# Kernel optimization log

Hardware: AMD Instinct MI355X
Metric: run time of the kernel (lower is better)

The kernel has to match this reference:

```python
import jax, jax.numpy as jnp
import numpy as np

N_USER = 100000
N_ITEM = 50000
N = N_USER + N_ITEM  # 150000 nodes
D = 64               # embedding_size
L = 3                # num_layers
E = 2000000          # edges
B = 8192             # batch of (user, item_p, item_n) triples
INT_W, POP_W, TIDE_W = 0.1, 0.1, 0.2


def setup_inputs() -> dict:
    key = jax.random.key(0)
    ks = jax.random.split(key, 10)
    stdv = 1.0 / np.sqrt(D)
    emb_int = jax.random.uniform(ks[0], (N, D), minval=-stdv, maxval=stdv, dtype=jnp.float32)
    emb_pop = jax.random.uniform(ks[1], (N, D), minval=-stdv, maxval=stdv, dtype=jnp.float32)
    q = jax.random.uniform(ks[2], (N_ITEM,), dtype=jnp.float32)
    b = jax.random.uniform(ks[3], (N_ITEM,), dtype=jnp.float32)
    user = jax.random.randint(ks[4], (B, 1), 0, N_USER)
    item_p = jax.random.randint(ks[5], (B, 1), 0, N_ITEM)
    item_n = jax.random.randint(ks[6], (B, 1), 0, N_ITEM)
    mask = jax.random.randint(ks[7], (B, 1), 0, 2).astype(bool)
    edge_src = jax.random.randint(ks[8], (E,), 0, N)
    edge_dst = jax.random.randint(ks[9], (E,), 0, N)
    return {"emb_int": emb_int, "emb_pop": emb_pop, "q": q, "b": b,
            "user": user, "item_p": item_p, "item_n": item_n, "mask": mask,
            "edge_src": edge_src, "edge_dst": edge_dst}


def reference(emb_int, emb_pop, q, b, user, item_p, item_n, mask, edge_src, edge_dst):
    # --- LightGCN symmetric normalization coefficients (per edge) ---
    ones = jnp.ones(edge_src.shape, emb_int.dtype)
    deg_out = jax.ops.segment_sum(ones, edge_src, num_segments=N)
    deg_in = jax.ops.segment_sum(ones, edge_dst, num_segments=N)
    norm = (jax.lax.rsqrt(jnp.maximum(deg_out, 1.0))[edge_src]
            * jax.lax.rsqrt(jnp.maximum(deg_in, 1.0))[edge_dst])  # [E]

    def propagate(e0):
        # L layers of LGConv (gather-scale-scatter), mean over layer outputs incl. layer 0.
        # Dropout is identity in eval mode (training=False).
        acc, h = e0, e0
        for _ in range(L):
            h = jax.ops.segment_sum(h[edge_src] * norm[:, None], edge_dst, num_segments=N)
            acc = acc + h
        return acc / (L + 1)

    f_int = propagate(emb_int)  # [N, D]
    f_pop = propagate(emb_pop)  # [N, D]

    ip = item_p + N_USER  # item node ids
    inn = item_n + N_USER
    u_i, u_p = f_int[user], f_pop[user]          # [B, 1, D]
    pi_i, pi_p = f_int[ip], f_pop[ip]
    ni_i, ni_p = f_int[inn], f_pop[inn]

    p_score_int = jnp.sum(u_i * pi_i, axis=2)    # [B, 1]
    n_score_int = jnp.sum(u_i * ni_i, axis=2)
    p_score_pop = jnp.sum(u_p * pi_p, axis=2)
    n_score_pop = jnp.sum(u_p * ni_p, axis=2)
    p_score_total = p_score_int + p_score_pop
    n_score_total = n_score_int + n_score_pop

    mf = mask.astype(p_score_int.dtype)
    nmf = (~mask).astype(p_score_int.dtype)

    def mask_bpr(p, n, m):
        return -jnp.mean(m * jax.nn.log_sigmoid(p - n))

    def bpr(p, n):
        return -jnp.mean(jax.nn.log_sigmoid(p - n))

    loss_int = mask_bpr(p_score_int, n_score_int, mf)
    loss_pop = mask_bpr(n_score_pop, p_score_pop, mf) - mask_bpr(p_score_pop, n_score_pop, nmf)

    pop_p = jax.nn.softplus(q[item_p]) + jax.nn.softplus(b[item_p])  # [B, 1]
    pop_n = jax.nn.softplus(q[item_n]) + jax.nn.softplus(b[item_n])
    loss_tide = bpr(jnp.tanh(pop_p) * p_score_total, jnp.tanh(pop_n) * n_score_total)

    return INT_W * loss_int + POP_W * loss_pop + TIDE_W * loss_tide
```

## Files before the change

kernel.cpp:

```cpp
#include <hip/hip_runtime.h>
#include <hip/hip_bf16.h>
#include <math.h>

#define N_USER 100000
#define N_ITEM 50000
#define NNODE  150000
#define DIM    64
#define NEDGE  2000000
#define BSZ    8192
#define NTGT   (3*BSZ)
#define CB     586
#define NB     512
#define CH     ((NEDGE + NB - 1)/NB)
#define LBLK   2048
#define PREPB  (NNODE*32/256)
#define CAP    5120

typedef float v2f __attribute__((ext_vector_type(2)));

__device__ __forceinline__ float logsigf(float x){
    return fminf(x, 0.f) - log1pf(expf(-fabsf(x)));
}
__device__ __forceinline__ float softplusf(float x){
    return fmaxf(x, 0.f) + log1pf(expf(-fabsf(x)));
}
__device__ __forceinline__ v2f fp8x2_to_f32(unsigned short u){
    return __builtin_amdgcn_cvt_pk_f32_fp8((int)u, false);
}
__device__ __forceinline__ unsigned short f32_to_fp8x2(float a, float b){
    return (unsigned short)__builtin_amdgcn_cvt_pk_fp8_f32(a, b, 0, false);
}
__device__ __forceinline__ unsigned rfl(unsigned v){
    return (unsigned)__builtin_amdgcn_readfirstlane((int)v);
}

__device__ __forceinline__ void scanCB(unsigned* arr, unsigned* tmp){
    int t = threadIdx.x;
    int base = 3*t;
    unsigned a0=0,a1=0,a2=0;
    if(base   < CB) a0 = arr[base];
    if(base+1 < CB) a1 = arr[base+1];
    if(base+2 < CB) a2 = arr[base+2];
    unsigned s = a0+a1+a2;
    tmp[t]=s; __syncthreads();
    for(int off=1; off<256; off<<=1){
        unsigned v = (t>=off)? tmp[t-off] : 0u;
        __syncthreads();
        tmp[t] += v;
        __syncthreads();
    }
    unsigned excl = tmp[t]-s;
    if(base   < CB) arr[base]   = excl;
    if(base+1 < CB) arr[base+1] = excl+a0;
    if(base+2 < CB) arr[base+2] = excl+a0+a1;
    __syncthreads();
}

__global__ __launch_bounds__(256) void k_hist(const int* __restrict__ src, const int* __restrict__ dst,
                       unsigned* __restrict__ histD, unsigned* __restrict__ histS,
                       const unsigned char* __restrict__ mask8, unsigned* __restrict__ mflag){
    if(blockIdx.x == NB){
        __shared__ int any;
        if(threadIdx.x==0) any=0;
        __syncthreads();
        for(int i=threadIdx.x;i<BSZ;i+=256){ if((i&3) && mask8[i]) any=1; }
        __syncthreads();
        if(threadIdx.x==0) *mflag = (any!=0) ? 1u : 0u;
        return;
    }
    __shared__ unsigned hD[CB], hS[CB];
    for(int i=threadIdx.x;i<CB;i+=256){ hD[i]=0; hS[i]=0; }
    __syncthreads();
    int lo = blockIdx.x*CH, hi = min(lo+CH, NEDGE);
    for(int e=lo+threadIdx.x; e<hi; e+=256){
        atomicAdd(&hS[src[e]>>8],1u);
        atomicAdd(&hD[dst[e]>>8],1u);
    }
    __syncthreads();
    for(int i=threadIdx.x;i<CB;i+=256){
        histD[(size_t)blockIdx.x*CB + i]=hD[i];
        histS[(size_t)blockIdx.x*CB + i]=hS[i];
    }
}

__global__ __launch_bounds__(512) void k_colscan(unsigned* __restrict__ histD, unsigned* __restrict__ histS,
                          unsigned* __restrict__ ctD, unsigned* __restrict__ ctS){
    unsigned* hist = blockIdx.y ? histS : histD;
    unsigned* ct   = blockIdx.y ? ctS   : ctD;
    int b = blockIdx.x;
    __shared__ unsigned sh[512];
    unsigned v = hist[(size_t)threadIdx.x*CB + b];
    sh[threadIdx.x] = v;
    __syncthreads();
    for(int off=1; off<512; off<<=1){
        unsigned t = (threadIdx.x>=off)? sh[threadIdx.x-off] : 0u;
        __syncthreads();
        sh[threadIdx.x] += t;
        __syncthreads();
    }
    hist[(size_t)threadIdx.x*CB + b] = sh[threadIdx.x] - v;
    if(threadIdx.x==511) ct[b] = sh[511];
}

__global__ __launch_bounds__(1024) void k_bstart(const unsigned* __restrict__ ctD, const unsigned* __restrict__ ctS,
                         unsigned* __restrict__ bsD, unsigned* __restrict__ bsS){
    __shared__ unsigned sh[1024];
    unsigned v = (threadIdx.x<CB)? ctD[threadIdx.x] : 0u;
    sh[threadIdx.x]=v; __syncthreads();
    for(int off=1; off<1024; off<<=1){ unsigned t=(threadIdx.x>=off)?sh[threadIdx.x-off]:0u; __syncthreads(); sh[threadIdx.x]+=t; __syncthreads(); }
    if(threadIdx.x<CB) bsD[threadIdx.x]=sh[threadIdx.x]-v;
    if(threadIdx.x==CB-1) bsD[CB]=sh[threadIdx.x];
    __syncthreads();
    unsigned v2 = (threadIdx.x<CB)? ctS[threadIdx.x] : 0u;
    sh[threadIdx.x]=v2; __syncthreads();
    for(int off=1; off<1024; off<<=1){ unsigned t=(threadIdx.x>=off)?sh[threadIdx.x-off]:0u; __syncthreads(); sh[threadIdx.x]+=t; __syncthreads(); }
    if(threadIdx.x<CB) bsS[threadIdx.x]=sh[threadIdx.x]-v2;
    if(threadIdx.x==CB-1) bsS[CB]=sh[threadIdx.x];
}

__global__ __launch_bounds__(256) void k_scatter(const int* __restrict__ src, const int* __restrict__ dst,
                          const unsigned* __restrict__ histD, const unsigned* __restrict__ histS,
                          const unsigned* __restrict__ bsD, const unsigned* __restrict__ bsS,
                          unsigned* __restrict__ part, unsigned char* __restrict__ spart){
    __shared__ unsigned curD[CB], curS[CB];
    __shared__ unsigned lhD[CB], lhS[CB];
    __shared__ unsigned startD[CB], startS[CB];
    __shared__ unsigned tmp[256];
    __shared__ unsigned partl[CH];
    __shared__ unsigned short keyD[CH];
    __shared__ unsigned short keyS[CH];
    __shared__ unsigned char sl[CH];
    for(int i=threadIdx.x;i<CB;i+=256){
        curD[i]=bsD[i]+histD[(size_t)blockIdx.x*CB+i];
        curS[i]=bsS[i]+histS[(size_t)blockIdx.x*CB+i];
        lhD[i]=0; lhS[i]=0;
    }
    __syncthreads();
    int lo=blockIdx.x*CH, hi=min(lo+CH,NEDGE);
    int n = hi-lo;
    for(int e=lo+threadIdx.x;e<hi;e+=256){
        atomicAdd(&lhD[dst[e]>>8],1u);
        atomicAdd(&lhS[src[e]>>8],1u);
    }
    __syncthreads();
    scanCB(lhD, tmp);
    scanCB(lhS, tmp);
    for(int i=threadIdx.x;i<CB;i+=256){ startD[i]=lhD[i]; startS[i]=lhS[i]; }
    __syncthreads();
    for(int e=lo+threadIdx.x;e<hi;e+=256){
        int s=src[e], d=dst[e];
        unsigned bd=(unsigned)(d>>8);
        unsigned slot=atomicAdd(&lhD[bd],1u);
        partl[slot]=((unsigned)(d&255)<<18)|(unsigned)s;
        keyD[slot]=(unsigned short)bd;
        unsigned bs=(unsigned)(s>>8);
        unsigned sslot=atomicAdd(&lhS[bs],1u);
        sl[sslot]=(unsigned char)(s&255);
        keyS[sslot]=(unsigned short)bs;
    }
    __syncthreads();
    for(int k=threadIdx.x;k<n;k+=256){
        unsigned b=keyD[k];
        part[curD[b] + (unsigned)k - startD[b]] = partl[k];
    }
    for(int k=threadIdx.x;k<n;k+=256){
        unsigned b=keyS[k];
        spart[curS[b] + (unsigned)k - startS[b]] = sl[k];
    }
}

__global__ __launch_bounds__(256) void k_degO(const unsigned char* __restrict__ spart, const unsigned* __restrict__ bsS,
                       float* __restrict__ rsqO, float* __restrict__ sqd){
    __shared__ unsigned cnt[256];
    cnt[threadIdx.x]=0;
    __syncthreads();
    unsigned lo=bsS[blockIdx.x], hi=bsS[blockIdx.x+1];
    for(unsigned e=lo+threadIdx.x;e<hi;e+=256) atomicAdd(&cnt[spart[e]],1u);
    __syncthreads();
    int node=(blockIdx.x<<8)+(int)threadIdx.x;
    if(node<NNODE){
        float dv = fmaxf((float)cnt[threadIdx.x],1.f);
        rsqO[node]=rsqrtf(dv);
        sqd[node]=sqrtf(dv)*0.125f;
    }
}

__global__ __launch_bounds__(256) void k_prep(const float2* __restrict__ ei, const float2* __restrict__ ep,
                      const float* __restrict__ rsqO,
                      unsigned* __restrict__ hE32, unsigned* __restrict__ h1g, unsigned* __restrict__ h2g,
                      unsigned* __restrict__ ecpad){
    if(blockIdx.x == PREPB){
        int t = threadIdx.x;
        if(t < 32) hE32[t] = 0u;
        else if(t < 64) h1g[t-32] = 0u;
        else if(t < 96) h2g[t-64] = 0u;
        else if(t < 160) ecpad[t-96] = 0u;
        return;
    }
    int idx = blockIdx.x*256 + threadIdx.x;
    int n = idx>>5, c = idx&31;
    float sc = 8.f*rsqO[n];
    float2 va, vb;
    if(c<16){ va = ei[(size_t)n*32 + 2*c]; vb = ei[(size_t)n*32 + 2*c+1]; }
    else    { va = ep[(size_t)n*32 + 2*c-32]; vb = ep[(size_t)n*32 + 2*c-31]; }
    int d = __builtin_amdgcn_cvt_pk_fp8_f32(va.x*sc, va.y*sc, 0, false);
    d = __builtin_amdgcn_cvt_pk_fp8_f32(vb.x*sc, vb.y*sc, d, true);
    hE32[32 + (size_t)n*32 + c] = (unsigned)d;
}

__global__ __launch_bounds__(256) void k_csr(const unsigned* __restrict__ part, const unsigned* __restrict__ bsD,
                      const float* __restrict__ rsqO,
                      unsigned* __restrict__ rs, unsigned* __restrict__ degI,
                      unsigned* __restrict__ ec, float* __restrict__ srow, float* __restrict__ rsqI8){
    __shared__ unsigned cnt[256], cur[256], sh[256];
    __shared__ unsigned partl[CAP];
    cnt[threadIdx.x]=0;
    __syncthreads();
    unsigned lo=bsD[blockIdx.x], hi=bsD[blockIdx.x+1];
    unsigned n = hi-lo;
    for(unsigned e=lo+threadIdx.x;e<hi;e+=256) atomicAdd(&cnt[part[e]>>18],1u);
    __syncthreads();
    unsigned c=cnt[threadIdx.x];
    sh[threadIdx.x]=c; __syncthreads();
    for(int o=1;o<256;o<<=1){ unsigned t=(threadIdx.x>=o)?sh[threadIdx.x-o]:0u; __syncthreads(); sh[threadIdx.x]+=t; __syncthreads(); }
    unsigned ex = sh[threadIdx.x]-c;
    cur[threadIdx.x]=ex;
    int node=(blockIdx.x<<8)+(int)threadIdx.x;
    if(node<NNODE){
        degI[node]=c; rs[node]=lo+ex;
        float rI = rsqrtf(fmaxf((float)c,1.f));
        float rO = rsqO[node];
        srow[node]  = rI*rO;
        rsqI8[node] = rI*0.125f;
    }
    __syncthreads();
    if(n <= CAP){
        for(unsigned e=lo+threadIdx.x;e<hi;e+=256){
            unsigned p=part[e];
            unsigned slot=atomicAdd(&cur[p>>18],1u);
            partl[slot]=p;
        }
        __syncthreads();
        for(unsigned k=threadIdx.x;k<n;k+=256){
            unsigned p=partl[k];
            ec[lo+k] = ((p&0x3FFFFu)+1u)<<7;
        }
    } else {
        for(unsigned e=lo+threadIdx.x;e<hi;e+=256){
            unsigned p=part[e];
            unsigned pos=lo+atomicAdd(&cur[p>>18],1u);
            ec[pos] = ((p&0x3FFFFu)+1u)<<7;
        }
    }
}

__device__ __forceinline__ void drain_row(const char* __restrict__ hb,
                                          const unsigned* __restrict__ ec,
                                          unsigned s, unsigned c, unsigned &i, unsigned lane2,
                                          v2f &acc){
    for(; i+4<=c; i+=4){
        unsigned e0=__builtin_nontemporal_load(&ec[s+i]);
        unsigned e1=__builtin_nontemporal_load(&ec[s+i+1]);
        unsigned e2=__builtin_nontemporal_load(&ec[s+i+2]);
        unsigned e3=__builtin_nontemporal_load(&ec[s+i+3]);
        unsigned short u0=*(const unsigned short*)(hb+e0+lane2);
        unsigned short u1=*(const unsigned short*)(hb+e1+lane2);
        unsigned short u2=*(const unsigned short*)(hb+e2+lane2);
        unsigned short u3=*(const unsigned short*)(hb+e3+lane2);
        acc += fp8x2_to_f32(u0); acc += fp8x2_to_f32(u1);
        acc += fp8x2_to_f32(u2); acc += fp8x2_to_f32(u3);
    }
    for(; i<c; ++i){
        unsigned e0=__builtin_nontemporal_load(&ec[s+i]);
        unsigned short u0=*(const unsigned short*)(hb+e0+lane2);
        acc += fp8x2_to_f32(u0);
    }
}

__global__ __launch_bounds__(256) void k_spmm_c(const unsigned short* __restrict__ hinb, unsigned short* __restrict__ houtb,
                                                const unsigned* __restrict__ rs, const unsigned* __restrict__ degI,
                                                const unsigned* __restrict__ ec, const float* __restrict__ srow){
    int wv = (blockIdx.x*256 + threadIdx.x) >> 6;
    int lane = threadIdx.x & 63;
    int r = 4*wv;
    if(r >= NNODE) return;
    unsigned s0=rfl(rs[r  ]), c0=rfl(degI[r  ]);
    unsigned s1=rfl(rs[r+1]), c1=rfl(degI[r+1]);
    unsigned s2=rfl(rs[r+2]), c2=rfl(degI[r+2]);
    unsigned s3=rfl(rs[r+3]), c3=rfl(degI[r+3]);
    const char* hb = (const char*)hinb;
    unsigned lane2 = ((unsigned)lane)*2u;
    v2f a0={0.f,0.f}, a1={0.f,0.f}, a2={0.f,0.f}, a3={0.f,0.f};
    unsigned i0=0,i1=0,i2=0,i3=0;
    while(i0+4<=c0 && i1+4<=c1 && i2+4<=c2 && i3+4<=c3){
        unsigned e00=__builtin_nontemporal_load(&ec[s0+i0]);
        unsigned e01=__builtin_nontemporal_load(&ec[s0+i0+1]);
        unsigned e02=__builtin_nontemporal_load(&ec[s0+i0+2]);
        unsigned e03=__builtin_nontemporal_load(&ec[s0+i0+3]);
        unsigned e10=__builtin_nontemporal_load(&ec[s1+i1]);
        unsigned e11=__builtin_nontemporal_load(&ec[s1+i1+1]);
        unsigned e12=__builtin_nontemporal_load(&ec[s1+i1+2]);
        unsigned e13=__builtin_nontemporal_load(&ec[s1+i1+3]);
        unsigned e20=__builtin_nontemporal_load(&ec[s2+i2]);
        unsigned e21=__builtin_nontemporal_load(&ec[s2+i2+1]);
        unsigned e22=__builtin_nontemporal_load(&ec[s2+i2+2]);
        unsigned e23=__builtin_nontemporal_load(&ec[s2+i2+3]);
        unsigned e30=__builtin_nontemporal_load(&ec[s3+i3]);
        unsigned e31=__builtin_nontemporal_load(&ec[s3+i3+1]);
        unsigned e32=__builtin_nontemporal_load(&ec[s3+i3+2]);
        unsigned e33=__builtin_nontemporal_load(&ec[s3+i3+3]);
        unsigned short u00=*(const unsigned short*)(hb+e00+lane2);
        unsigned short u01=*(const unsigned short*)(hb+e01+lane2);
        unsigned short u02=*(const unsigned short*)(hb+e02+lane2);
        unsigned short u03=*(const unsigned short*)(hb+e03+lane2);
        unsigned short u10=*(const unsigned short*)(hb+e10+lane2);
        unsigned short u11=*(const unsigned short*)(hb+e11+lane2);
        unsigned short u12=*(const unsigned short*)(hb+e12+lane2);
        unsigned short u13=*(const unsigned short*)(hb+e13+lane2);
        unsigned short u20=*(const unsigned short*)(hb+e20+lane2);
        unsigned short u21=*(const unsigned short*)(hb+e21+lane2);
        unsigned short u22=*(const unsigned short*)(hb+e22+lane2);
        unsigned short u23=*(const unsigned short*)(hb+e23+lane2);
        unsigned short u30=*(const unsigned short*)(hb+e30+lane2);
        unsigned short u31=*(const unsigned short*)(hb+e31+lane2);
        unsigned short u32v=*(const unsigned short*)(hb+e32+lane2);
        unsigned short u33=*(const unsigned short*)(hb+e33+lane2);
        a0 += fp8x2_to_f32(u00); a0 += fp8x2_to_f32(u01); a0 += fp8x2_to_f32(u02); a0 += fp8x2_to_f32(u03);
        a1 += fp8x2_to_f32(u10); a1 += fp8x2_to_f32(u11); a1 += fp8x2_to_f32(u12); a1 += fp8x2_to_f32(u13);
        a2 += fp8x2_to_f32(u20); a2 += fp8x2_to_f32(u21); a2 += fp8x2_to_f32(u22); a2 += fp8x2_to_f32(u23);
        a3 += fp8x2_to_f32(u30); a3 += fp8x2_to_f32(u31); a3 += fp8x2_to_f32(u32v); a3 += fp8x2_to_f32(u33);
        i0+=4; i1+=4; i2+=4; i3+=4;
    }
    drain_row(hb, ec, s0, c0, i0, lane2, a0);
    drain_row(hb, ec, s1, c1, i1, lane2, a1);
    drain_row(hb, ec, s2, c2, i2, lane2, a2);
    drain_row(hb, ec, s3, c3, i3, lane2, a3);
    float sc0=srow[r], sc1=srow[r+1], sc2=srow[r+2], sc3=srow[r+3];
    houtb[(size_t)(r+1)*64+lane] = f32_to_fp8x2(sc0*a0.x, sc0*a0.y);
    houtb[(size_t)(r+2)*64+lane] = f32_to_fp8x2(sc1*a1.x, sc1*a1.y);
    houtb[(size_t)(r+3)*64+lane] = f32_to_fp8x2(sc2*a2.x, sc2*a2.y);
    houtb[(size_t)(r+4)*64+lane] = f32_to_fp8x2(sc3*a3.x, sc3*a3.y);
}

__global__ __launch_bounds__(256) void k_spmm_t(const unsigned short* __restrict__ hinb, float2* __restrict__ h3,
                                                const unsigned* __restrict__ rs, const unsigned* __restrict__ degI,
                                                const unsigned* __restrict__ ec, const float* __restrict__ rsqI8,
                                                const int* __restrict__ user, const int* __restrict__ itp,
                                                const int* __restrict__ itn){
    int wv = (blockIdx.x*256 + threadIdx.x) >> 6;
    int lane = threadIdx.x & 63;
    int t0 = 2*wv, t1 = 2*wv+1;
    if(t0 >= NTGT) return;
    int sec0 = t0>>13, b0 = t0&(BSZ-1);
    int sec1 = t1>>13, b1 = t1&(BSZ-1);
    int n0 = (sec0==0) ? user[b0] : ((sec0==1) ? itp[b0]+N_USER : itn[b0]+N_USER);
    int n1 = (sec1==0) ? user[b1] : ((sec1==1) ? itp[b1]+N_USER : itn[b1]+N_USER);
    n0 = __builtin_amdgcn_readfirstlane(n0);
    n1 = __builtin_amdgcn_readfirstlane(n1);
    unsigned s0 = rfl(rs[n0]), c0 = rfl(degI[n0]);
    unsigned s1 = rfl(rs[n1]), c1 = rfl(degI[n1]);
    const char* hb = (const char*)hinb;
    unsigned lane2 = ((unsigned)lane)*2u;
    v2f a0={0.f,0.f}, a1={0.f,0.f};
    unsigned i0=0, i1=0;
    while(i0+4<=c0 && i1+4<=c1){
        unsigned e0=__builtin_nontemporal_load(&ec[s0+i0]);
        unsigned e1=__builtin_nontemporal_load(&ec[s0+i0+1]);
        unsigned e2=__builtin_nontemporal_load(&ec[s0+i0+2]);
        unsigned e3=__builtin_nontemporal_load(&ec[s0+i0+3]);
        unsigned e4=__builtin_nontemporal_load(&ec[s1+i1]);
        unsigned e5=__builtin_nontemporal_load(&ec[s1+i1+1]);
        unsigned e6=__builtin_nontemporal_load(&ec[s1+i1+2]);
        unsigned e7=__builtin_nontemporal_load(&ec[s1+i1+3]);
        unsigned short u0=*(const unsigned short*)(hb+e0+lane2);
        unsigned short u1=*(const unsigned short*)(hb+e1+lane2);
        unsigned short u2=*(const unsigned short*)(hb+e2+lane2);
        unsigned short u3=*(const unsigned short*)(hb+e3+lane2);
        unsigned short u4=*(const unsigned short*)(hb+e4+lane2);
        unsigned short u5=*(const unsigned short*)(hb+e5+lane2);
        unsigned short u6=*(const unsigned short*)(hb+e6+lane2);
        unsigned short u7=*(const unsigned short*)(hb+e7+lane2);
        a0 += fp8x2_to_f32(u0); a0 += fp8x2_to_f32(u1); a0 += fp8x2_to_f32(u2); a0 += fp8x2_to_f32(u3);
        a1 += fp8x2_to_f32(u4); a1 += fp8x2_to_f32(u5); a1 += fp8x2_to_f32(u6); a1 += fp8x2_to_f32(u7);
        i0+=4; i1+=4;
    }
    drain_row(hb, ec, s0, c0, i0, lane2, a0);
    drain_row(hb, ec, s1, c1, i1, lane2, a1);
    float t0s = rsqI8[n0], t1s = rsqI8[n1];
    h3[(size_t)t0*64+lane] = make_float2(a0.x*t0s, a0.y*t0s);
    h3[(size_t)t1*64+lane] = make_float2(a1.x*t1s, a1.y*t1s);
}

__global__ __launch_bounds__(256) void k_scoreloss(const float2* __restrict__ ei, const float2* __restrict__ ep,
                        const unsigned short* __restrict__ h1C, const unsigned short* __restrict__ h2C,
                        const float2* __restrict__ h3,
                        const float* __restrict__ q, const float* __restrict__ bq,
                        const int* __restrict__ user, const int* __restrict__ item_p, const int* __restrict__ item_n,
                        const void* __restrict__ mask, const unsigned* __restrict__ mflag,
                        const float* __restrict__ sqd,
                        float4* __restrict__ partial){
    int t = blockIdx.x*256 + threadIdx.x;
    int b = t >> 6, l = t & 63;
    int wv = threadIdx.x >> 6;
    __shared__ float4 wsum[4];
    int nu = user[b];
    int np = item_p[b] + N_USER;
    int nn = item_n[b] + N_USER;

    float2 e0u, e0p, e0n;
    if(l < 32){
        e0u = ei[(size_t)nu*32 + l]; e0p = ei[(size_t)np*32 + l]; e0n = ei[(size_t)nn*32 + l];
    } else {
        e0u = ep[(size_t)nu*32 + (l-32)]; e0p = ep[(size_t)np*32 + (l-32)]; e0n = ep[(size_t)nn*32 + (l-32)];
    }
    v2f h1u = fp8x2_to_f32(h1C[(size_t)(nu+1)*64 + l]);
    v2f h1p = fp8x2_to_f32(h1C[(size_t)(np+1)*64 + l]);
    v2f h1n = fp8x2_to_f32(h1C[(size_t)(nn+1)*64 + l]);
    v2f h2u = fp8x2_to_f32(h2C[(size_t)(nu+1)*64 + l]);
    v2f h2p = fp8x2_to_f32(h2C[(size_t)(np+1)*64 + l]);
    v2f h2n = fp8x2_to_f32(h2C[(size_t)(nn+1)*64 + l]);
    float2 h3u = h3[(size_t)b*64 + l];
    float2 h3p = h3[(size_t)(BSZ   + b)*64 + l];
    float2 h3n = h3[(size_t)(2*BSZ + b)*64 + l];

    float squ = sqd[nu], sqp = sqd[np], sqn = sqd[nn];

    float fux = e0u.x + squ*(h1u.x + h2u.x) + h3u.x, fuy = e0u.y + squ*(h1u.y + h2u.y) + h3u.y;
    float fpx = e0p.x + sqp*(h1p.x + h2p.x) + h3p.x, fpy = e0p.y + sqp*(h1p.y + h2p.y) + h3p.y;
    float fnx = e0n.x + sqn*(h1n.x + h2n.x) + h3n.x, fny = e0n.y + sqn*(h1n.y + h2n.y) + h3n.y;

    float dp = fux*fpx + fuy*fpy;
    float dn = fux*fnx + fuy*fny;
    for(int off=16; off; off>>=1){ dp += __shfl_down(dp,off,32); dn += __shfl_down(dn,off,32); }
    float pi  = __shfl(dp, 0, 64) * (1.f/16.f);
    float ni  = __shfl(dn, 0, 64) * (1.f/16.f);
    float pp  = __shfl(dp, 32, 64) * (1.f/16.f);
    float npp = __shfl(dn, 32, 64) * (1.f/16.f);
    if(l == 0){
        bool bytes = (*mflag)!=0;
        float mf = bytes ? (((const unsigned char*)mask)[b]?1.f:0.f)
                         : (((const int*)mask)[b]?1.f:0.f);
        float nmf = 1.f-mf;
        float a0 = mf  * logsigf(pi-ni);
        float a1 = mf  * logsigf(npp-pp);
        float a2 = nmf * logsigf(pp-npp);
        int ip=item_p[b], in_=item_n[b];
        float popp = softplusf(q[ip]) + softplusf(bq[ip]);
        float popn = softplusf(q[in_]) + softplusf(bq[in_]);
        float a3 = logsigf(tanhf(popp)*(pi+pp) - tanhf(popn)*(ni+npp));
        wsum[wv] = make_float4(a0,a1,a2,a3);
    }
    __syncthreads();
    if(threadIdx.x == 0){
        float4 s0=wsum[0], s1=wsum[1], s2=wsum[2], s3=wsum[3];
        partial[blockIdx.x] = make_float4(s0.x+s1.x+s2.x+s3.x, s0.y+s1.y+s2.y+s3.y,
                                          s0.z+s1.z+s2.z+s3.z, s0.w+s1.w+s2.w+s3.w);
    }
}

__global__ __launch_bounds__(256) void k_lossfin(const float4* __restrict__ partial, float* __restrict__ out){
    __shared__ float4 sh[256];
    float4 s = make_float4(0,0,0,0);
    for(int i=threadIdx.x; i<LBLK; i+=256){
        float4 v = partial[i];
        s.x+=v.x; s.y+=v.y; s.z+=v.z; s.w+=v.w;
    }
    sh[threadIdx.x]=s;
    __syncthreads();
    for(int off=128; off; off>>=1){
        if(threadIdx.x < off){
            float4 a=sh[threadIdx.x], b2=sh[threadIdx.x+off];
            sh[threadIdx.x]=make_float4(a.x+b2.x,a.y+b2.y,a.z+b2.z,a.w+b2.w);
        }
        __syncthreads();
    }
    if(threadIdx.x==0){
        const float invB = 1.f/(float)BSZ;
        float4 t = sh[0];
        float loss_int  = -t.x*invB;
        float loss_pop  = -t.y*invB + t.z*invB;
        float loss_tide = -t.w*invB;
        out[0] = 0.1f*loss_int + 0.1f*loss_pop + 0.2f*loss_tide;
    }
}

extern "C" void kernel_launch(void* const* d_in, const int* in_sizes, int n_in,
                              void* d_out, int out_size, void* d_ws, size_t ws_size,
                              hipStream_t stream){
    const float* emb_int = (const float*)d_in[0];
    const float* emb_pop = (const float*)d_in[1];
    const float* q    = (const float*)d_in[2];
    const float* bq   = (const float*)d_in[3];
    const int* user   = (const int*)d_in[4];
    const int* item_p = (const int*)d_in[5];
    const int* item_n = (const int*)d_in[6];
    const void* mask  = d_in[7];
    const int* esrc   = (const int*)d_in[8];
    const int* edst   = (const int*)d_in[9];

    char* ws = (char*)d_ws;
    size_t o = 0;
    auto take = [&](size_t bytes)->char*{ char* p = ws + o; o = (o + bytes + 255) & ~(size_t)255; return p; };
    unsigned* histD = (unsigned*)take((size_t)NB*CB*4);
    unsigned* histS = (unsigned*)take((size_t)NB*CB*4);
    unsigned* ctD   = (unsigned*)take((size_t)CB*4);
    unsigned* ctS   = (unsigned*)take((size_t)CB*4);
    unsigned* bsD   = (unsigned*)take((size_t)(CB+1)*4);
    unsigned* bsS   = (unsigned*)take((size_t)(CB+1)*4);
    unsigned* part  = (unsigned*)take((size_t)NEDGE*4);
    unsigned char* spart = (unsigned char*)take((size_t)NEDGE);
    float*    rsqO  = (float*)take((size_t)NNODE*4);
    float*    sqd   = (float*)take((size_t)NNODE*4);
    unsigned* rs    = (unsigned*)take((size_t)NNODE*4);
    unsigned* degI  = (unsigned*)take((size_t)NNODE*4);
    unsigned* ec    = (unsigned*)take((size_t)NEDGE*4 + 256);
    float*    srow  = (float*)take((size_t)NNODE*4);
    float*    rsqI8 = (float*)take((size_t)NNODE*4);
    unsigned short* hEb  = (unsigned short*)take((size_t)(NNODE+1)*64*2);
    unsigned short* h1Cb = (unsigned short*)take((size_t)(NNODE+1)*64*2);
    unsigned short* h2Cb = (unsigned short*)take((size_t)(NNODE+1)*64*2);
    float2*   h3    = (float2*)take((size_t)NTGT*64*8);
    float4*   partial = (float4*)take((size_t)LBLK*16);
    unsigned* mflag = (unsigned*)take(256);
    (void)ws_size; (void)in_sizes; (void)n_in; (void)out_size;

    k_hist<<<NB+1,256,0,stream>>>(esrc, edst, histD, histS,
                                  (const unsigned char*)mask, mflag);
    k_colscan<<<dim3(CB,2),512,0,stream>>>(histD, histS, ctD, ctS);
    k_bstart<<<1,1024,0,stream>>>(ctD, ctS, bsD, bsS);
    k_scatter<<<NB,256,0,stream>>>(esrc, edst, histD, histS, bsD, bsS, part, spart);
    k_degO<<<CB,256,0,stream>>>(spart, bsS, rsqO, sqd);
    k_csr<<<CB,256,0,stream>>>(part, bsD, rsqO, rs, degI, ec, srow, rsqI8);
    k_prep<<<PREPB+1,256,0,stream>>>((const float2*)emb_int, (const float2*)emb_pop, rsqO,
                                     (unsigned*)hEb, (unsigned*)h1Cb, (unsigned*)h2Cb,
                                     ec + NEDGE);

    const int spB = ((NNODE/4)*64 + 255)/256;
    k_spmm_c<<<spB,256,0,stream>>>(hEb,  h1Cb, rs, degI, ec, srow);
    k_spmm_c<<<spB,256,0,stream>>>(h1Cb, h2Cb, rs, degI, ec, srow);
    k_spmm_t<<<((NTGT/2)*64 + 255)/256,256,0,stream>>>(h2Cb, h3, rs, degI, ec, rsqI8,
                                                 user, item_p, item_n);
    k_scoreloss<<<LBLK,256,0,stream>>>((const float2*)emb_int, (const float2*)emb_pop,
                                       h1Cb, h2Cb, h3, q, bq, user, item_p, item_n,
                                       mask, mflag, sqd, partial);
    k_lossfin<<<1,256,0,stream>>>(partial, (float*)d_out);
}
```

Before: 336.9 us.

## Pad CSR rows to multiples of four for vectorized index loads; widen histogram grid

The CSR builder now pads every row's edge list to a multiple of four with zero entries that point at the zero padding row. Each row segment is aligned to 16 bytes, and a per-block slack region absorbs the padding. The SpMM kernels can then fetch four edge indices with a single 128-bit nontemporal load and drop the scalar tail loop. The histogram pass also uses four times as many blocks, and the column scan handles four entries per thread to match. In exchange, k_csr gains a second scan and the padding writes, and the edge-index buffer grows.

```diff
diff --git a/kernel.cpp b/kernel.cpp
--- a/kernel.cpp
+++ b/kernel.cpp
@@ -10,13 +10,15 @@
 #define BSZ    8192
 #define NTGT   (3*BSZ)
 #define CB     586
-#define NB     512
+#define NB     2048
 #define CH     ((NEDGE + NB - 1)/NB)
 #define LBLK   2048
 #define PREPB  (NNODE*32/256)
 #define CAP    5120
+#define BSLACK 772
 
 typedef float v2f __attribute__((ext_vector_type(2)));
+typedef unsigned v4u __attribute__((ext_vector_type(4)));
 
 __device__ __forceinline__ float logsigf(float x){
     return fminf(x, 0.f) - log1pf(expf(-fabsf(x)));
@@ -32,6 +34,9 @@
 }
 __device__ __forceinline__ unsigned rfl(unsigned v){
     return (unsigned)__builtin_amdgcn_readfirstlane((int)v);
+}
+__device__ __forceinline__ v4u nt4(const unsigned* p){
+    return __builtin_nontemporal_load((const v4u*)p);
 }
 
 __device__ __forceinline__ void scanCB(unsigned* arr, unsigned* tmp){
@@ -88,18 +93,27 @@
     unsigned* hist = blockIdx.y ? histS : histD;
     unsigned* ct   = blockIdx.y ? ctS   : ctD;
     int b = blockIdx.x;
+    int t = threadIdx.x;
     __shared__ unsigned sh[512];
-    unsigned v = hist[(size_t)threadIdx.x*CB + b];
-    sh[threadIdx.x] = v;
+    unsigned v0 = hist[(size_t)(4*t  )*CB + b];
+    unsigned v1 = hist[(size_t)(4*t+1)*CB + b];
+    unsigned v2 = hist[(size_t)(4*t+2)*CB + b];
+    unsigned v3 = hist[(size_t)(4*t+3)*CB + b];
+    unsigned s = v0+v1+v2+v3;
+    sh[t] = s;
     __syncthreads();
     for(int off=1; off<512; off<<=1){
-        unsigned t = (threadIdx.x>=off)? sh[threadIdx.x-off] : 0u;
-        __syncthreads();
-        sh[threadIdx.x] += t;
-        __syncthreads();
-    }
-    hist[(size_t)threadIdx.x*CB + b] = sh[threadIdx.x] - v;
-    if(threadIdx.x==511) ct[b] = sh[511];
+        unsigned u = (t>=off)? sh[t-off] : 0u;
+        __syncthreads();
+        sh[t] += u;
+        __syncthreads();
+    }
+    unsigned e = sh[t] - s;
+    hist[(size_t)(4*t  )*CB + b] = e;
+    hist[(size_t)(4*t+1)*CB + b] = e+v0;
+    hist[(size_t)(4*t+2)*CB + b] = e+v0+v1;
+    hist[(size_t)(4*t+3)*CB + b] = e+v0+v1+v2;
+    if(t==511) ct[b] = e+s;
 }
 
 __global__ __launch_bounds__(1024) void k_bstart(const unsigned* __restrict__ ctD, const unsigned* __restrict__ ctS,
@@ -187,14 +201,12 @@
 
 __global__ __launch_bounds__(256) void k_prep(const float2* __restrict__ ei, const float2* __restrict__ ep,
                       const float* __restrict__ rsqO,
-                      unsigned* __restrict__ hE32, unsigned* __restrict__ h1g, unsigned* __restrict__ h2g,
-                      unsigned* __restrict__ ecpad){
+                      unsigned* __restrict__ hE32, unsigned* __restrict__ h1g, unsigned* __restrict__ h2g){
     if(blockIdx.x == PREPB){
         int t = threadIdx.x;
         if(t < 32) hE32[t] = 0u;
         else if(t < 64) h1g[t-32] = 0u;
         else if(t < 96) h2g[t-64] = 0u;
-        else if(t < 160) ecpad[t-96] = 0u;
         return;
     }
     int idx = blockIdx.x*256 + threadIdx.x;
@@ -213,6 +225,7 @@
                       unsigned* __restrict__ rs, unsigned* __restrict__ degI,
                       unsigned* __restrict__ ec, float* __restrict__ srow, float* __restrict__ rsqI8){
     __shared__ unsigned cnt[256], cur[256], sh[256];
+    __shared__ unsigned stR[256], exR[256];
     __shared__ unsigned partl[CAP];
     cnt[threadIdx.x]=0;
     __syncthreads();
@@ -221,18 +234,26 @@
     for(unsigned e=lo+threadIdx.x;e<hi;e+=256) atomicAdd(&cnt[part[e]>>18],1u);
     __syncthreads();
     unsigned c=cnt[threadIdx.x];
+    unsigned r4=(c+3u)&~3u;
     sh[threadIdx.x]=c; __syncthreads();
     for(int o=1;o<256;o<<=1){ unsigned t=(threadIdx.x>=o)?sh[threadIdx.x-o]:0u; __syncthreads(); sh[threadIdx.x]+=t; __syncthreads(); }
     unsigned ex = sh[threadIdx.x]-c;
-    cur[threadIdx.x]=ex;
+    __syncthreads();
+    sh[threadIdx.x]=r4; __syncthreads();
+    for(int o=1;o<256;o<<=1){ unsigned t=(threadIdx.x>=o)?sh[threadIdx.x-o]:0u; __syncthreads(); sh[threadIdx.x]+=t; __syncthreads(); }
+    unsigned ex_r = sh[threadIdx.x]-r4;
+    stR[threadIdx.x]=ex; exR[threadIdx.x]=ex_r;
+    cur[threadIdx.x]=(n<=CAP)? ex : ex_r;
+    unsigned lo_ec = ((lo+3u)&~3u) + (unsigned)BSLACK*blockIdx.x;
     int node=(blockIdx.x<<8)+(int)threadIdx.x;
     if(node<NNODE){
-        degI[node]=c; rs[node]=lo+ex;
+        degI[node]=r4; rs[node]=lo_ec+ex_r;
         float rI = rsqrtf(fmaxf((float)c,1.f));
         float rO = rsqO[node];
         srow[node]  = rI*rO;
         rsqI8[node] = rI*0.125f;
     }
+    for(unsigned j=c;j<r4;++j) ec[lo_ec+ex_r+j]=0u;
     __syncthreads();
     if(n <= CAP){
         for(unsigned e=lo+threadIdx.x;e<hi;e+=256){
@@ -243,37 +264,30 @@
         __syncthreads();
         for(unsigned k=threadIdx.x;k<n;k+=256){
             unsigned p=partl[k];
-            ec[lo+k] = ((p&0x3FFFFu)+1u)<<7;
+            unsigned fb=p>>18;
+            ec[lo_ec + exR[fb] + (k - stR[fb])] = ((p&0x3FFFFu)+1u)<<7;
         }
     } else {
         for(unsigned e=lo+threadIdx.x;e<hi;e+=256){
             unsigned p=part[e];
-            unsigned pos=lo+atomicAdd(&cur[p>>18],1u);
+            unsigned pos=lo_ec+atomicAdd(&cur[p>>18],1u);
             ec[pos] = ((p&0x3FFFFu)+1u)<<7;
         }
     }
 }
 
-__device__ __forceinline__ void drain_row(const char* __restrict__ hb,
-                                          const unsigned* __restrict__ ec,
-                                          unsigned s, unsigned c, unsigned &i, unsigned lane2,
-                                          v2f &acc){
+__device__ __forceinline__ void drain4(const char* __restrict__ hb,
+                                       const unsigned* __restrict__ ec,
+                                       unsigned s, unsigned c, unsigned &i, unsigned lane2,
+                                       v2f &acc){
     for(; i+4<=c; i+=4){
-        unsigned e0=__builtin_nontemporal_load(&ec[s+i]);
-        unsigned e1=__builtin_nontemporal_load(&ec[s+i+1]);
-        unsigned e2=__builtin_nontemporal_load(&ec[s+i+2]);
-        unsigned e3=__builtin_nontemporal_load(&ec[s+i+3]);
-        unsigned short u0=*(const unsigned short*)(hb+e0+lane2);
-        unsigned short u1=*(const unsigned short*)(hb+e1+lane2);
-        unsigned short u2=*(const unsigned short*)(hb+e2+lane2);
-        unsigned short u3=*(const unsigned short*)(hb+e3+lane2);
+        v4u e = nt4(&ec[s+i]);
+        unsigned short u0=*(const unsigned short*)(hb+e.x+lane2);
+        unsigned short u1=*(const unsigned short*)(hb+e.y+lane2);
+        unsigned short u2=*(const unsigned short*)(hb+e.z+lane2);
+        unsigned short u3=*(const unsigned short*)(hb+e.w+lane2);
         acc += fp8x2_to_f32(u0); acc += fp8x2_to_f32(u1);
         acc += fp8x2_to_f32(u2); acc += fp8x2_to_f32(u3);
-    }
-    for(; i<c; ++i){
-        unsigned e0=__builtin_nontemporal_load(&ec[s+i]);
-        unsigned short u0=*(const unsigned short*)(hb+e0+lane2);
-        acc += fp8x2_to_f32(u0);
     }
 }
 
@@ -293,48 +307,36 @@
     v2f a0={0.f,0.f}, a1={0.f,0.f}, a2={0.f,0.f}, a3={0.f,0.f};
     unsigned i0=0,i1=0,i2=0,i3=0;
     while(i0+4<=c0 && i1+4<=c1 && i2+4<=c2 && i3+4<=c3){
-        unsigned e00=__builtin_nontemporal_load(&ec[s0+i0]);
-        unsigned e01=__builtin_nontemporal_load(&ec[s0+i0+1]);
-        unsigned e02=__builtin_nontemporal_load(&ec[s0+i0+2]);
-        unsigned e03=__builtin_nontemporal_load(&ec[s0+i0+3]);
-        unsigned e10=__builtin_nontemporal_load(&ec[s1+i1]);
-        unsigned e11=__builtin_nontemporal_load(&ec[s1+i1+1]);
-        unsigned e12=__builtin_nontemporal_load(&ec[s1+i1+2]);
-        unsigned e13=__builtin_nontemporal_load(&ec[s1+i1+3]);
-        unsigned e20=__builtin_nontemporal_load(&ec[s2+i2]);
-        unsigned e21=__builtin_nontemporal_load(&ec[s2+i2+1]);
-        unsigned e22=__builtin_nontemporal_load(&ec[s2+i2+2]);
-        unsigned e23=__builtin_nontemporal_load(&ec[s2+i2+3]);
-        unsigned e30=__builtin_nontemporal_load(&ec[s3+i3]);
-        unsigned e31=__builtin_nontemporal_load(&ec[s3+i3+1]);
-        unsigned e32=__builtin_nontemporal_load(&ec[s3+i3+2]);
-        unsigned e33=__builtin_nontemporal_load(&ec[s3+i3+3]);
-        unsigned short u00=*(const unsigned short*)(hb+e00+lane2);
-        unsigned short u01=*(const unsigned short*)(hb+e01+lane2);
-        unsigned short u02=*(const unsigned short*)(hb+e02+lane2);
-        unsigned short u03=*(const unsigned short*)(hb+e03+lane2);
-        unsigned short u10=*(const unsigned short*)(hb+e10+lane2);
-        unsigned short u11=*(const unsigned short*)(hb+e11+lane2);
-        unsigned short u12=*(const unsigned short*)(hb+e12+lane2);
-        unsigned short u13=*(const unsigned short*)(hb+e13+lane2);
-        unsigned short u20=*(const unsigned short*)(hb+e20+lane2);
-        unsigned short u21=*(const unsigned short*)(hb+e21+lane2);
-        unsigned short u22=*(const unsigned short*)(hb+e22+lane2);
-        unsigned short u23=*(const unsigned short*)(hb+e23+lane2);
-        unsigned short u30=*(const unsigned short*)(hb+e30+lane2);
-        unsigned short u31=*(const unsigned short*)(hb+e31+lane2);
-        unsigned short u32v=*(const unsigned short*)(hb+e32+lane2);
-        unsigned short u33=*(const unsigned short*)(hb+e33+lane2);
+        v4u eA = nt4(&ec[s0+i0]);
+        v4u eB = nt4(&ec[s1+i1]);
+        v4u eC = nt4(&ec[s2+i2]);
+        v4u eD = nt4(&ec[s3+i3]);
+        unsigned short u00=*(const unsigned short*)(hb+eA.x+lane2);
+        unsigned short u01=*(const unsigned short*)(hb+eA.y+lane2);
+        unsigned short u02=*(const unsigned short*)(hb+eA.z+lane2);
+        unsigned short u03=*(const unsigned short*)(hb+eA.w+lane2);
+        unsigned short u10=*(const unsigned short*)(hb+eB.x+lane2);
+        unsigned short u11=*(const unsigned short*)(hb+eB.y+lane2);
+        unsigned short u12=*(const unsigned short*)(hb+eB.z+lane2);
+        unsigned short u13=*(const unsigned short*)(hb+eB.w+lane2);
+        unsigned short u20=*(const unsigned short*)(hb+eC.x+lane2);
+        unsigned short u21=*(const unsigned short*)(hb+eC.y+lane2);
+        unsigned short u22=*(const unsigned short*)(hb+eC.z+lane2);
+        unsigned short u23=*(const unsigned short*)(hb+eC.w+lane2);
+        unsigned short u30=*(const unsigned short*)(hb+eD.x+lane2);
+        unsigned short u31=*(const unsigned short*)(hb+eD.y+lane2);
+        unsigned short u32v=*(const unsigned short*)(hb+eD.z+lane2);
+        unsigned short u33=*(const unsigned short*)(hb+eD.w+lane2);
         a0 += fp8x2_to_f32(u00); a0 += fp8x2_to_f32(u01); a0 += fp8x2_to_f32(u02); a0 += fp8x2_to_f32(u03);
         a1 += fp8x2_to_f32(u10); a1 += fp8x2_to_f32(u11); a1 += fp8x2_to_f32(u12); a1 += fp8x2_to_f32(u13);
         a2 += fp8x2_to_f32(u20); a2 += fp8x2_to_f32(u21); a2 += fp8x2_to_f32(u22); a2 += fp8x2_to_f32(u23);
         a3 += fp8x2_to_f32(u30); a3 += fp8x2_to_f32(u31); a3 += fp8x2_to_f32(u32v); a3 += fp8x2_to_f32(u33);
         i0+=4; i1+=4; i2+=4; i3+=4;
     }
-    drain_row(hb, ec, s0, c0, i0, lane2, a0);
-    drain_row(hb, ec, s1, c1, i1, lane2, a1);
-    drain_row(hb, ec, s2, c2, i2, lane2, a2);
-    drain_row(hb, ec, s3, c3, i3, lane2, a3);
+    drain4(hb, ec, s0, c0, i0, lane2, a0);
+    drain4(hb, ec, s1, c1, i1, lane2, a1);
+    drain4(hb, ec, s2, c2, i2, lane2, a2);
+    drain4(hb, ec, s3, c3, i3, lane2, a3);
     float sc0=srow[r], sc1=srow[r+1], sc2=srow[r+2], sc3=srow[r+3];
     houtb[(size_t)(r+1)*64+lane] = f32_to_fp8x2(sc0*a0.x, sc0*a0.y);
     houtb[(size_t)(r+2)*64+lane] = f32_to_fp8x2(sc1*a1.x, sc1*a1.y);
@@ -364,28 +366,22 @@
     v2f a0={0.f,0.f}, a1={0.f,0.f};
     unsigned i0=0, i1=0;
     while(i0+4<=c0 && i1+4<=c1){
-        unsigned e0=__builtin_nontemporal_load(&ec[s0+i0]);
-        unsigned e1=__builtin_nontemporal_load(&ec[s0+i0+1]);
-        unsigned e2=__builtin_nontemporal_load(&ec[s0+i0+2]);
-        unsigned e3=__builtin_nontemporal_load(&ec[s0+i0+3]);
-        unsigned e4=__builtin_nontemporal_load(&ec[s1+i1]);
-        unsigned e5=__builtin_nontemporal_load(&ec[s1+i1+1]);
-        unsigned e6=__builtin_nontemporal_load(&ec[s1+i1+2]);
-        unsigned e7=__builtin_nontemporal_load(&ec[s1+i1+3]);
-        unsigned short u0=*(const unsigned short*)(hb+e0+lane2);
-        unsigned short u1=*(const unsigned short*)(hb+e1+lane2);
-        unsigned short u2=*(const unsigned short*)(hb+e2+lane2);
-        unsigned short u3=*(const unsigned short*)(hb+e3+lane2);
-        unsigned short u4=*(const unsigned short*)(hb+e4+lane2);
-        unsigned short u5=*(const unsigned short*)(hb+e5+lane2);
-        unsigned short u6=*(const unsigned short*)(hb+e6+lane2);
-        unsigned short u7=*(const unsigned short*)(hb+e7+lane2);
+        v4u eA = nt4(&ec[s0+i0]);
+        v4u eB = nt4(&ec[s1+i1]);
+        unsigned short u0=*(const unsigned short*)(hb+eA.x+lane2);
+        unsigned short u1=*(const unsigned short*)(hb+eA.y+lane2);
+        unsigned short u2=*(const unsigned short*)(hb+eA.z+lane2);
+        unsigned short u3=*(const unsigned short*)(hb+eA.w+lane2);
+        unsigned short u4=*(const unsigned short*)(hb+eB.x+lane2);
+        unsigned short u5=*(const unsigned short*)(hb+eB.y+lane2);
+        unsigned short u6=*(const unsigned short*)(hb+eB.z+lane2);
+        unsigned short u7=*(const unsigned short*)(hb+eB.w+lane2);
         a0 += fp8x2_to_f32(u0); a0 += fp8x2_to_f32(u1); a0 += fp8x2_to_f32(u2); a0 += fp8x2_to_f32(u3);
         a1 += fp8x2_to_f32(u4); a1 += fp8x2_to_f32(u5); a1 += fp8x2_to_f32(u6); a1 += fp8x2_to_f32(u7);
         i0+=4; i1+=4;
     }
-    drain_row(hb, ec, s0, c0, i0, lane2, a0);
-    drain_row(hb, ec, s1, c1, i1, lane2, a1);
+    drain4(hb, ec, s0, c0, i0, lane2, a0);
+    drain4(hb, ec, s1, c1, i1, lane2, a1);
     float t0s = rsqI8[n0], t1s = rsqI8[n1];
     h3[(size_t)t0*64+lane] = make_float2(a0.x*t0s, a0.y*t0s);
     h3[(size_t)t1*64+lane] = make_float2(a1.x*t1s, a1.y*t1s);
@@ -513,7 +509,7 @@
     float*    sqd   = (float*)take((size_t)NNODE*4);
     unsigned* rs    = (unsigned*)take((size_t)NNODE*4);
     unsigned* degI  = (unsigned*)take((size_t)NNODE*4);
-    unsigned* ec    = (unsigned*)take((size_t)NEDGE*4 + 256);
+    unsigned* ec    = (unsigned*)take((size_t)(NEDGE + BSLACK*CB + 16)*4);
     float*    srow  = (float*)take((size_t)NNODE*4);
     float*    rsqI8 = (float*)take((size_t)NNODE*4);
     unsigned short* hEb  = (unsigned short*)take((size_t)(NNODE+1)*64*2);
@@ -532,8 +528,7 @@
     k_degO<<<CB,256,0,stream>>>(spart, bsS, rsqO, sqd);
     k_csr<<<CB,256,0,stream>>>(part, bsD, rsqO, rs, degI, ec, srow, rsqI8);
     k_prep<<<PREPB+1,256,0,stream>>>((const float2*)emb_int, (const float2*)emb_pop, rsqO,
-                                     (unsigned*)hEb, (unsigned*)h1Cb, (unsigned*)h2Cb,
-                                     ec + NEDGE);
+                                     (unsigned*)hEb, (unsigned*)h1Cb, (unsigned*)h2Cb);
 
     const int spB = ((NNODE/4)*64 + 255)/256;
     k_spmm_c<<<spB,256,0,stream>>>(hEb,  h1Cb, rs, degI, ec, srow);
```

Measured after the change: 364.6 us. 8.2% more time.
